# Optimization experiments

Hardware: AMD Instinct MI355X
Metric: run time of the kernel (lower is better)

The kernel has to match this reference:

```python
import jax, jax.numpy as jnp
import numpy as np

N_NODES = 4096
N_EDGES = 32768
IN_FEAT = 256
OUT_FEAT = 128
HID = 64
IN_HEAD = 64
OUT_HEAD = 5
NEG_SLOPE = 0.2
EPS = 1e-16


def setup_inputs() -> dict:
    key = jax.random.key(0)
    ks = jax.random.split(key, 12)
    x = jax.random.normal(ks[0], (N_NODES, IN_FEAT), dtype=jnp.float32)
    src = jax.random.randint(ks[1], (N_EDGES,), 0, N_NODES)
    dst = jax.random.randint(ks[2], (N_EDGES,), 0, N_NODES)
    edge_index = jnp.stack([src, dst]).astype(jnp.int64)
    s1 = 1.0 / np.sqrt(IN_FEAT)
    s2 = 1.0 / np.sqrt(HID * IN_HEAD)
    W1 = jax.random.normal(ks[3], (IN_FEAT, IN_HEAD * HID), dtype=jnp.float32) * s1
    att_src1 = jax.random.normal(ks[4], (IN_HEAD, HID), dtype=jnp.float32) * 0.1
    att_dst1 = jax.random.normal(ks[5], (IN_HEAD, HID), dtype=jnp.float32) * 0.1
    b1 = jnp.zeros((IN_HEAD * HID,), dtype=jnp.float32)
    W2 = jax.random.normal(ks[6], (IN_HEAD * HID, OUT_HEAD * OUT_FEAT), dtype=jnp.float32) * s2
    att_src2 = jax.random.normal(ks[7], (OUT_HEAD, OUT_FEAT), dtype=jnp.float32) * 0.1
    att_dst2 = jax.random.normal(ks[8], (OUT_HEAD, OUT_FEAT), dtype=jnp.float32) * 0.1
    b2 = jnp.zeros((OUT_FEAT,), dtype=jnp.float32)
    return {"x": x, "edge_index": edge_index, "W1": W1, "att_src1": att_src1,
            "att_dst1": att_dst1, "b1": b1, "W2": W2, "att_src2": att_src2,
            "att_dst2": att_dst2, "b2": b2}


def _gat_conv(x, W, att_src, att_dst, bias, src, dst, heads, out_c, concat):
    # x: [N, F_in]; returns [N, heads*out_c] (concat) or [N, out_c] (mean)
    n = x.shape[0]
    h = (x @ W).reshape(n, heads, out_c)                       # [N,H,C]
    a_src = jnp.sum(h * att_src, axis=-1)                      # [N,H]
    a_dst = jnp.sum(h * att_dst, axis=-1)                      # [N,H]
    e = jax.nn.leaky_relu(a_src[src] + a_dst[dst], NEG_SLOPE)  # [E,H]
    # segment softmax over edges grouped by destination node (PyG softmax)
    m = jax.ops.segment_max(e, dst, num_segments=n)            # [N,H]
    ex = jnp.exp(e - m[dst])
    denom = jax.ops.segment_sum(ex, dst, num_segments=n)       # [N,H]
    alpha = ex / (denom[dst] + EPS)                            # [E,H]
    out = jax.ops.segment_sum(alpha[:, :, None] * h[src], dst, num_segments=n)  # [N,H,C]
    out = out.reshape(n, heads * out_c) if concat else out.mean(axis=1)
    return out + bias


def reference(x, edge_index, W1, att_src1, att_dst1, b1, W2, att_src2, att_dst2, b2):
    n = x.shape[0]
    # PyG GATConv default: add self loops
    loop = jnp.arange(n, dtype=edge_index.dtype)
    src = jnp.concatenate([edge_index[0], loop])
    dst = jnp.concatenate([edge_index[1], loop])
    # dropout layers are identity in eval mode
    h = _gat_conv(x, W1, att_src1, att_dst1, b1, src, dst, IN_HEAD, HID, True)
    h = jax.nn.elu(h)
    h = _gat_conv(h, W2, att_src2, att_dst2, b2, src, dst, OUT_HEAD, OUT_FEAT, False)
    s = jnp.mean(h, axis=0)
    return jnp.tanh(s)
```

## Files before the change

### kernel.cpp

```cpp
#include <hip/hip_runtime.h>
#include <hip/hip_bf16.h>

#define N_NODES 4096
#define NE      32768
#define E_TOT   (NE + N_NODES)
#define IN_FEAT 256
#define HID     64
#define IN_HEAD 64
#define F1      4096
#define OUT_HEAD 5
#define OUT_FEAT 128
#define F2      640
#define NEG_SLOPE 0.2f
#define EPS_A   1e-16f

typedef __bf16 bf16;
typedef bf16 bf16x8 __attribute__((ext_vector_type(8)));
typedef bf16 bf16x4 __attribute__((ext_vector_type(4)));
typedef float f32x4 __attribute__((ext_vector_type(4)));

__device__ inline void async_cp16(bf16* lds, const bf16* g) {
    __builtin_amdgcn_global_load_lds(
        (const __attribute__((address_space(1))) unsigned int*)g,
        (__attribute__((address_space(3))) unsigned int*)lds, 16, 0, 0);
}

__global__ void hist_kernel(const int* __restrict__ edst, int* counts) {
    int e = blockIdx.x * 256 + threadIdx.x;
    if (e >= E_TOT) return;
    int d = (e < NE) ? edst[e] : (e - NE);
    atomicAdd(&counts[d], 1);
}

__global__ void scan_kernel(const int* __restrict__ counts,
                            int* __restrict__ row_start, int* __restrict__ cursor) {
    __shared__ int part[256];
    __shared__ int pre[257];
    int t = threadIdx.x;
    int base = t * 16;
    int local[16];
    int s = 0;
#pragma unroll
    for (int i = 0; i < 16; ++i) { local[i] = s; s += counts[base + i]; }
    part[t] = s;
    __syncthreads();
    if (t == 0) {
        int r = 0;
        for (int i = 0; i < 256; ++i) { pre[i] = r; r += part[i]; }
        pre[256] = r;
    }
    __syncthreads();
    int off = pre[t];
#pragma unroll
    for (int i = 0; i < 16; ++i) {
        int v = off + local[i];
        row_start[base + i] = v;
        cursor[base + i] = v;
    }
    if (t == 0) row_start[N_NODES] = pre[256];
}

__global__ void scatter_kernel(const int* __restrict__ edst,
                               int* cursor, int* __restrict__ elist) {
    int e = blockIdx.x * 256 + threadIdx.x;
    if (e >= E_TOT) return;
    int d = (e < NE) ? edst[e] : (e - NE);
    int slot = atomicAdd(&cursor[d], 1);
    elist[slot] = e;
}

#define PB_X   512
#define PB_W1  1024
#define PB_W2  2560
__global__ __launch_bounds__(256)
void prep_kernel(const float* __restrict__ x, bf16* __restrict__ xb,
                 const float* __restrict__ W1, bf16* __restrict__ W1T,
                 const float* __restrict__ W2, bf16* __restrict__ W2T,
                 const float* __restrict__ as1, const float* __restrict__ ad1,
                 bf16* __restrict__ w1s, bf16* __restrict__ w1d) {
    __shared__ float tile[32][33];
    int b = blockIdx.x, t = threadIdx.x;
    if (b < PB_X) {
        int i = b * 256 + t;
        f32x4 a = *(const f32x4*)(x + (size_t)i * 8);
        f32x4 c = *(const f32x4*)(x + (size_t)i * 8 + 4);
        bf16x8 r;
        r[0] = (bf16)a[0]; r[1] = (bf16)a[1]; r[2] = (bf16)a[2]; r[3] = (bf16)a[3];
        r[4] = (bf16)c[0]; r[5] = (bf16)c[1]; r[6] = (bf16)c[2]; r[7] = (bf16)c[3];
        *(bf16x8*)(xb + (size_t)i * 8) = r;
    } else if (b < PB_X + PB_W1 + PB_W2) {
        const float* S; bf16* D; int R, C, gx, gy;
        if (b < PB_X + PB_W1) {
            int bb = b - PB_X;
            S = W1; D = W1T; R = IN_FEAT; C = F1;
            gx = bb % (F1 / 32); gy = bb / (F1 / 32);
        } else {
            int bb = b - PB_X - PB_W1;
            S = W2; D = W2T; R = F1; C = F2;
            gx = bb % (F2 / 32); gy = bb / (F2 / 32);
        }
        int tx = t & 31, ty = t >> 5;
        int c0 = gx * 32, r0 = gy * 32;
#pragma unroll
        for (int i = 0; i < 4; ++i)
            tile[ty + i * 8][tx] = S[(size_t)(r0 + ty + i * 8) * C + c0 + tx];
        __syncthreads();
#pragma unroll
        for (int i = 0; i < 4; ++i)
            D[(size_t)(c0 + ty + i * 8) * R + r0 + tx] = (bf16)tile[tx][ty + i * 8];
    } else {
        int id = (b - PB_X - PB_W1 - PB_W2) * 256 + t;
        int k = id >> 6, h = id & 63;
        const float* wrow = W1 + (size_t)k * F1 + h * HID;
        const float* a1 = as1 + h * HID;
        const float* a2 = ad1 + h * HID;
        float s = 0.f, d = 0.f;
#pragma unroll 8
        for (int c = 0; c < HID; ++c) {
            float w = wrow[c];
            s += w * a1[c];
            d += w * a2[c];
        }
        w1s[id] = (bf16)s;
        w1d[id] = (bf16)d;
    }
}

template <int SPLITK, bool SWZ, typename TC>
__global__ __launch_bounds__(256)
void gemm128_kernel(const bf16* __restrict__ A, const bf16* __restrict__ BT,
                    TC* __restrict__ C, int M, int N, int K) {
    __shared__ bf16 As[128][64];
    __shared__ bf16 Bs[128][64];
    const int tid  = threadIdx.x;
    const int wave = tid >> 6, lane = tid & 63;
    const int quad = lane >> 4, lr = lane & 15;
    int nb, mb, zb;
    if constexpr (SWZ) {
        int bid = blockIdx.x;
        int xx = bid & 7, q = bid >> 3;
        int gp = q / 5; nb = q - gp * 5;
        int g = gp * 8 + xx;
        mb = g >> 2; zb = g & 3;
    } else {
        nb = blockIdx.x; mb = blockIdx.y; zb = blockIdx.z;
    }
    const int m0 = mb * 128, n0 = nb * 128;
    const int kchunk = K / SPLITK;
    const int kbeg = zb * kchunk;
    const int wm = (wave >> 1) * 64;
    const int wn = (wave & 1) * 64;
    TC* Cz = C + (size_t)zb * M * N;

    const int srow = lane >> 3;
    const int scol = ((lane & 7) ^ srow) * 8;
    const int xk = lr & 7;

    f32x4 acc[4][4] = {};

    for (int kk = 0; kk < kchunk; kk += 64) {
        int k0 = kbeg + kk;
#pragma unroll
        for (int c = 0; c < 4; ++c) {
            int r = wave * 32 + c * 8;
            async_cp16(&As[r][0], A + (size_t)(m0 + r + srow) * K + k0 + scol);
            async_cp16(&Bs[r][0], BT + (size_t)(n0 + r + srow) * K + k0 + scol);
        }
        __syncthreads();

#pragma unroll
        for (int ks = 0; ks < 2; ++ks) {
            int ch = ((ks * 4 + quad) ^ xk) * 8;
            bf16x8 af[4], bfr[4];
#pragma unroll
            for (int mt = 0; mt < 4; ++mt)
                af[mt] = *(const bf16x8*)(&As[wm + mt * 16 + lr][ch]);
#pragma unroll
            for (int nt = 0; nt < 4; ++nt)
                bfr[nt] = *(const bf16x8*)(&Bs[wn + nt * 16 + lr][ch]);
#pragma unroll
            for (int mt = 0; mt < 4; ++mt)
#pragma unroll
                for (int nt = 0; nt < 4; ++nt)
                    acc[mt][nt] = __builtin_amdgcn_mfma_f32_16x16x32_bf16(
                        af[mt], bfr[nt], acc[mt][nt], 0, 0, 0);
        }
        __syncthreads();
    }

#pragma unroll
    for (int mt = 0; mt < 4; ++mt)
#pragma unroll
        for (int nt = 0; nt < 4; ++nt) {
            int row0 = m0 + wm + mt * 16 + quad * 4;
            int col = n0 + wn + nt * 16 + lr;
#pragma unroll
            for (int r = 0; r < 4; ++r)
                Cz[(size_t)(row0 + r) * N + col] = (TC)acc[mt][nt][r];
        }
}

__global__ __launch_bounds__(256)
void gemv1_kernel(const float* __restrict__ x,
                  const bf16* __restrict__ w1s, const bf16* __restrict__ w1d,
                  float* __restrict__ a_src, float* __restrict__ a_dst) {
    int wave = threadIdx.x >> 6, lane = threadIdx.x & 63;
    int n = blockIdx.x * 4 + wave;
    const float* xr = x + (size_t)n * IN_FEAT;
    float s = 0.f, d = 0.f;
    for (int k0 = 0; k0 < IN_FEAT; k0 += 4) {
        f32x4 xv = *(const f32x4*)(xr + k0);
#pragma unroll
        for (int j = 0; j < 4; ++j) {
            float xs = xv[j];
            s += xs * (float)w1s[(k0 + j) * IN_HEAD + lane];
            d += xs * (float)w1d[(k0 + j) * IN_HEAD + lane];
        }
    }
    a_src[n * IN_HEAD + lane] = s;
    a_dst[n * IN_HEAD + lane] = d;
}

__global__ __launch_bounds__(64)
void agg1_kernel(const int* __restrict__ es, const int* __restrict__ row_start,
                 const int* __restrict__ elist,
                 const float* __restrict__ a_src, const float* __restrict__ a_dst,
                 const bf16* __restrict__ H1, const float* __restrict__ b1,
                 bf16* __restrict__ h_elu) {
    int bid = blockIdx.x;
    int c = bid & 7;
    int d = bid >> 3;
    int lane = threadIdx.x;
    int gh = c * 8 + (lane >> 3);
    int beg = row_start[d], deg = row_start[d + 1] - beg;
    float adst = a_dst[d * IN_HEAD + gh];
    int fbase = c * 512 + lane * 8;

    float m = -1e30f, den = 0.f;
    float acc[8] = {};
    for (int i = 0; i < deg; ++i) {
        int e = elist[beg + i];
        int s = (e < NE) ? es[e] : d;
        float l = a_src[s * IN_HEAD + gh] + adst;
        l = l > 0.f ? l : NEG_SLOPE * l;
        if (l > m + 12.f) {
            float r = __expf(m - l);
            den *= r;
#pragma unroll
            for (int k = 0; k < 8; ++k) acc[k] *= r;
            m = l;
        }
        float w = __expf(l - m);
        den += w;
        bf16x8 v = *(const bf16x8*)(H1 + (size_t)s * F1 + fbase);
#pragma unroll
        for (int k = 0; k < 8; ++k) acc[k] += w * (float)v[k];
    }
    float dinv = 1.f / (den + EPS_A);

    bf16x8 o;
#pragma unroll
    for (int j = 0; j < 8; ++j) {
        float v = acc[j] * dinv + b1[fbase + j];
        o[j] = (bf16)(v > 0.f ? v : (__expf(v) - 1.f));
    }
    *(bf16x8*)(h_elu + (size_t)d * F1 + fbase) = o;
}

__global__ __launch_bounds__(192)
void fold2_kernel(const bf16* __restrict__ Hp,
                  const float* __restrict__ as2, const float* __restrict__ ad2,
                  float* __restrict__ H2,
                  float* __restrict__ a_src, float* __restrict__ a_dst) {
    int n = blockIdx.x, t = threadIdx.x;
    if (t >= 160) return;
    int h = t >> 5;
    f32x4 sum = {};
#pragma unroll
    for (int z = 0; z < 4; ++z) {
        bf16x4 v = *(const bf16x4*)(Hp + (size_t)z * N_NODES * F2 + (size_t)n * F2 + t * 4);
        sum[0] += (float)v[0]; sum[1] += (float)v[1];
        sum[2] += (float)v[2]; sum[3] += (float)v[3];
    }
    *(f32x4*)(H2 + (size_t)n * F2 + t * 4) = sum;
    f32x4 ws = *(const f32x4*)(as2 + t * 4);
    f32x4 wd = *(const f32x4*)(ad2 + t * 4);
    float s = sum[0] * ws[0] + sum[1] * ws[1] + sum[2] * ws[2] + sum[3] * ws[3];
    float d = sum[0] * wd[0] + sum[1] * wd[1] + sum[2] * wd[2] + sum[3] * wd[3];
#pragma unroll
    for (int o = 1; o <= 16; o <<= 1) {
        s += __shfl_xor(s, o);
        d += __shfl_xor(d, o);
    }
    if ((t & 31) == 0) {
        a_src[n * OUT_HEAD + h] = s;
        a_dst[n * OUT_HEAD + h] = d;
    }
}

__global__ void stats2_kernel(const int* __restrict__ es,
                              const int* __restrict__ row_start,
                              const int* __restrict__ elist,
                              const float* __restrict__ a_src,
                              const float* __restrict__ a_dst,
                              float* __restrict__ m2, float* __restrict__ dinv2) {
    int id = blockIdx.x * 256 + threadIdx.x;
    if (id >= N_NODES * OUT_HEAD) return;
    int d = id / OUT_HEAD, h = id - d * OUT_HEAD;
    int beg = row_start[d], deg = row_start[d + 1] - beg;
    float adst = a_dst[id];
    float m = -1e30f, den = 0.f;
    for (int i = 0; i < deg; ++i) {
        int e = elist[beg + i];
        int s = (e < NE) ? es[e] : d;
        float l = a_src[s * OUT_HEAD + h] + adst;
        l = l > 0.f ? l : NEG_SLOPE * l;
        if (l > m) { den = den * __expf(m - l) + 1.f; m = l; }
        else den += __expf(l - m);
    }
    m2[id] = m;
    dinv2[id] = 1.f / (den + EPS_A);
}

__global__ void beta_kernel(const int* __restrict__ es, const int* __restrict__ ed,
                            const float* __restrict__ a_src, const float* __restrict__ a_dst,
                            const float* __restrict__ m2, const float* __restrict__ dinv2,
                            float* __restrict__ beta) {
    int id = blockIdx.x * 256 + threadIdx.x;
    if (id >= E_TOT * OUT_HEAD) return;
    int e = id / OUT_HEAD, h = id - e * OUT_HEAD;
    int s = (e < NE) ? es[e] : (e - NE);
    int d = (e < NE) ? ed[e] : (e - NE);
    float l = a_src[s * OUT_HEAD + h] + a_dst[d * OUT_HEAD + h];
    l = l > 0.f ? l : NEG_SLOPE * l;
    float alpha = __expf(l - m2[d * OUT_HEAD + h]) * dinv2[d * OUT_HEAD + h];
    atomicAdd(&beta[s * OUT_HEAD + h], alpha);
}

__global__ __launch_bounds__(256)
void wsum_kernel(const float* __restrict__ H2, const float* __restrict__ beta,
                 float* __restrict__ acc_out) {
    __shared__ float buf[F2];
    int t = threadIdx.x;
    int n0 = blockIdx.x * 32;
    int h = t >> 5;
    float a0 = 0.f, a1 = 0.f, a2 = 0.f, a3 = 0.f;
    if (t < 160) {
        for (int i = 0; i < 32; ++i) {
            int s = n0 + i;
            float bh = beta[s * OUT_HEAD + h];
            f32x4 v = *(const f32x4*)(H2 + (size_t)s * F2 + t * 4);
            a0 += bh * v[0]; a1 += bh * v[1];
            a2 += bh * v[2]; a3 += bh * v[3];
        }
        buf[t * 4 + 0] = a0; buf[t * 4 + 1] = a1;
        buf[t * 4 + 2] = a2; buf[t * 4 + 3] = a3;
    }
    __syncthreads();
    if (t < OUT_FEAT) {
        float s = 0.f;
#pragma unroll
        for (int hh = 0; hh < OUT_HEAD; ++hh) s += buf[hh * OUT_FEAT + t];
        atomicAdd(&acc_out[(blockIdx.x & 7) * OUT_FEAT + t], s);
    }
}

__global__ void tanh_kernel(const float* __restrict__ acc_out,
                            const float* __restrict__ b2, float* __restrict__ out) {
    int c = threadIdx.x;
    float tot = 0.f;
#pragma unroll
    for (int k = 0; k < 8; ++k) tot += acc_out[k * OUT_FEAT + c];
    out[c] = tanhf(tot * (1.f / (OUT_HEAD * (float)N_NODES)) + b2[c]);
}

extern "C" void kernel_launch(void* const* d_in, const int* in_sizes, int n_in,
                              void* d_out, int out_size, void* d_ws, size_t ws_size,
                              hipStream_t stream) {
    const float* x        = (const float*)d_in[0];
    const int*   ei       = (const int*)d_in[1];
    const float* W1       = (const float*)d_in[2];
    const float* att_src1 = (const float*)d_in[3];
    const float* att_dst1 = (const float*)d_in[4];
    const float* b1       = (const float*)d_in[5];
    const float* W2       = (const float*)d_in[6];
    const float* att_src2 = (const float*)d_in[7];
    const float* att_dst2 = (const float*)d_in[8];
    const float* b2       = (const float*)d_in[9];
    float* out = (float*)d_out;

    const int* esrc = ei;
    const int* edst = ei + NE;

    char* p = (char*)d_ws;
    auto bump = [&](size_t bytes) {
        void* r = (void*)p;
        p += (bytes + 255) & ~(size_t)255;
        return r;
    };
    bf16*  H1     = (bf16*)bump((size_t)N_NODES * F1 * 2);
    bf16*  h_elu  = (bf16*)bump((size_t)N_NODES * F1 * 2);
    float* H2     = (float*)bump((size_t)N_NODES * F2 * 4);
    bf16*  xb     = (bf16*)bump((size_t)N_NODES * IN_FEAT * 2);
    bf16*  W1T    = (bf16*)bump((size_t)F1 * IN_FEAT * 2);
    bf16*  W2T    = (bf16*)bump((size_t)F2 * F1 * 2);
    bf16*  w1s    = (bf16*)bump((size_t)IN_FEAT * IN_HEAD * 2);
    bf16*  w1d    = (bf16*)bump((size_t)IN_FEAT * IN_HEAD * 2);
    float* a_src1 = (float*)bump((size_t)N_NODES * IN_HEAD * 4);
    float* a_dst1 = (float*)bump((size_t)N_NODES * IN_HEAD * 4);
    float* a_src2 = (float*)bump((size_t)N_NODES * OUT_HEAD * 4);
    float* a_dst2 = (float*)bump((size_t)N_NODES * OUT_HEAD * 4);
    float* m2     = (float*)bump((size_t)N_NODES * OUT_HEAD * 4);
    float* dinv2  = (float*)bump((size_t)N_NODES * OUT_HEAD * 4);
    int*   row_start = (int*)bump((N_NODES + 1) * 4);
    int*   cursor = (int*)bump(N_NODES * 4);
    int*   elist  = (int*)bump(E_TOT * 4);
    int*   counts = (int*)bump(N_NODES * 4 + N_NODES * OUT_HEAD * 4 + 8 * OUT_FEAT * 4);
    float* beta    = (float*)((char*)counts + N_NODES * 4);
    float* acc_out = beta + N_NODES * OUT_HEAD;
    bf16* Hp = H1;

    hipMemsetAsync(counts, 0,
                   N_NODES * 4 + N_NODES * OUT_HEAD * 4 + 8 * OUT_FEAT * 4, stream);

    hist_kernel<<<(E_TOT + 255) / 256, 256, 0, stream>>>(edst, counts);
    scan_kernel<<<1, 256, 0, stream>>>(counts, row_start, cursor);
    scatter_kernel<<<(E_TOT + 255) / 256, 256, 0, stream>>>(edst, cursor, elist);

    prep_kernel<<<PB_X + PB_W1 + PB_W2 + 64, 256, 0, stream>>>(
        x, xb, W1, W1T, W2, W2T, att_src1, att_dst1, w1s, w1d);

    gemm128_kernel<1, false, bf16>
        <<<dim3(F1 / 128, N_NODES / 128, 1), 256, 0, stream>>>(
        xb, W1T, H1, N_NODES, F1, IN_FEAT);
    gemv1_kernel<<<N_NODES / 4, 256, 0, stream>>>(x, w1s, w1d, a_src1, a_dst1);
    agg1_kernel<<<N_NODES * 8, 64, 0, stream>>>(
        esrc, row_start, elist, a_src1, a_dst1, H1, b1, h_elu);

    gemm128_kernel<4, true, bf16><<<640, 256, 0, stream>>>(
        h_elu, W2T, Hp, N_NODES, F2, F1);
    fold2_kernel<<<N_NODES, 192, 0, stream>>>(
        Hp, att_src2, att_dst2, H2, a_src2, a_dst2);
    stats2_kernel<<<(N_NODES * OUT_HEAD + 255) / 256, 256, 0, stream>>>(
        esrc, row_start, elist, a_src2, a_dst2, m2, dinv2);
    beta_kernel<<<(E_TOT * OUT_HEAD + 255) / 256, 256, 0, stream>>>(
        esrc, edst, a_src2, a_dst2, m2, dinv2, beta);
    wsum_kernel<<<N_NODES / 32, 256, 0, stream>>>(H2, beta, acc_out);

    tanh_kernel<<<1, OUT_FEAT, 0, stream>>>(acc_out, b2, out);
}
```

Baseline: 252.3 us.

## Store source ids in CSR, prefetch agg1 gathers, fuse beta and tanh kernels

The scatter step now writes source node ids into the CSR list instead of edge ids, which removes one level of indirection in agg1 and stats2. agg1 adds a software pipeline that loads a_src and the H1 rows up to three edges ahead to hide gather latency. The beta kernel is folded into stats2 as a second pass over each node's edges, and the final tanh kernel is folded into wsum using a last-block ticket. Two launches go away, at the cost of more registers in agg1 and more serial per-thread work in stats2.

```diff
diff --git a/kernel.cpp b/kernel.cpp
--- a/kernel.cpp
+++ b/kernel.cpp
@@ -60,13 +60,15 @@
     if (t == 0) row_start[N_NODES] = pre[256];
 }
 
-__global__ void scatter_kernel(const int* __restrict__ edst,
-                               int* cursor, int* __restrict__ elist) {
+__global__ void scatter_kernel(const int* __restrict__ esrc,
+                               const int* __restrict__ edst,
+                               int* cursor, int* __restrict__ srclist) {
     int e = blockIdx.x * 256 + threadIdx.x;
     if (e >= E_TOT) return;
     int d = (e < NE) ? edst[e] : (e - NE);
+    int s = (e < NE) ? esrc[e] : (e - NE);
     int slot = atomicAdd(&cursor[d], 1);
-    elist[slot] = e;
+    srclist[slot] = s;
 }
 
 #define PB_X   512
@@ -222,8 +224,8 @@
 }
 
 __global__ __launch_bounds__(64)
-void agg1_kernel(const int* __restrict__ es, const int* __restrict__ row_start,
-                 const int* __restrict__ elist,
+void agg1_kernel(const int* __restrict__ row_start,
+                 const int* __restrict__ srclist,
                  const float* __restrict__ a_src, const float* __restrict__ a_dst,
                  const bf16* __restrict__ H1, const float* __restrict__ b1,
                  bf16* __restrict__ h_elu) {
@@ -235,13 +237,26 @@
     int beg = row_start[d], deg = row_start[d + 1] - beg;
     float adst = a_dst[d * IN_HEAD + gh];
     int fbase = c * 512 + lane * 8;
+    const float* asg = a_src + gh;
+
+    auto SL = [&](int i) { return srclist[beg + (i < deg ? i : deg - 1)]; };
+
+    int s0 = SL(0);
+    int s1 = SL(1);
+    float la0 = asg[(size_t)s0 * IN_HEAD];
+    bf16x8 v0 = *(const bf16x8*)(H1 + (size_t)s0 * F1 + fbase);
+    float la1 = asg[(size_t)s1 * IN_HEAD];
+    bf16x8 v1 = *(const bf16x8*)(H1 + (size_t)s1 * F1 + fbase);
+    int s2 = SL(2);
 
     float m = -1e30f, den = 0.f;
     float acc[8] = {};
     for (int i = 0; i < deg; ++i) {
-        int e = elist[beg + i];
-        int s = (e < NE) ? es[e] : d;
-        float l = a_src[s * IN_HEAD + gh] + adst;
+        int s3 = SL(i + 3);
+        float la2 = asg[(size_t)s2 * IN_HEAD];
+        bf16x8 v2 = *(const bf16x8*)(H1 + (size_t)s2 * F1 + fbase);
+
+        float l = la0 + adst;
         l = l > 0.f ? l : NEG_SLOPE * l;
         if (l > m + 12.f) {
             float r = __expf(m - l);
@@ -252,9 +267,12 @@
         }
         float w = __expf(l - m);
         den += w;
-        bf16x8 v = *(const bf16x8*)(H1 + (size_t)s * F1 + fbase);
-#pragma unroll
-        for (int k = 0; k < 8; ++k) acc[k] += w * (float)v[k];
+#pragma unroll
+        for (int k = 0; k < 8; ++k) acc[k] += w * (float)v0[k];
+
+        la0 = la1; v0 = v1;
+        la1 = la2; v1 = v2;
+        s2 = s3;
     }
     float dinv = 1.f / (den + EPS_A);
 
@@ -298,12 +316,11 @@
     }
 }
 
-__global__ void stats2_kernel(const int* __restrict__ es,
-                              const int* __restrict__ row_start,
-                              const int* __restrict__ elist,
+__global__ void stats2_kernel(const int* __restrict__ row_start,
+                              const int* __restrict__ srclist,
                               const float* __restrict__ a_src,
                               const float* __restrict__ a_dst,
-                              float* __restrict__ m2, float* __restrict__ dinv2) {
+                              float* __restrict__ beta) {
     int id = blockIdx.x * 256 + threadIdx.x;
     if (id >= N_NODES * OUT_HEAD) return;
     int d = id / OUT_HEAD, h = id - d * OUT_HEAD;
@@ -311,36 +328,27 @@
     float adst = a_dst[id];
     float m = -1e30f, den = 0.f;
     for (int i = 0; i < deg; ++i) {
-        int e = elist[beg + i];
-        int s = (e < NE) ? es[e] : d;
+        int s = srclist[beg + i];
         float l = a_src[s * OUT_HEAD + h] + adst;
         l = l > 0.f ? l : NEG_SLOPE * l;
         if (l > m) { den = den * __expf(m - l) + 1.f; m = l; }
         else den += __expf(l - m);
     }
-    m2[id] = m;
-    dinv2[id] = 1.f / (den + EPS_A);
-}
-
-__global__ void beta_kernel(const int* __restrict__ es, const int* __restrict__ ed,
-                            const float* __restrict__ a_src, const float* __restrict__ a_dst,
-                            const float* __restrict__ m2, const float* __restrict__ dinv2,
-                            float* __restrict__ beta) {
-    int id = blockIdx.x * 256 + threadIdx.x;
-    if (id >= E_TOT * OUT_HEAD) return;
-    int e = id / OUT_HEAD, h = id - e * OUT_HEAD;
-    int s = (e < NE) ? es[e] : (e - NE);
-    int d = (e < NE) ? ed[e] : (e - NE);
-    float l = a_src[s * OUT_HEAD + h] + a_dst[d * OUT_HEAD + h];
-    l = l > 0.f ? l : NEG_SLOPE * l;
-    float alpha = __expf(l - m2[d * OUT_HEAD + h]) * dinv2[d * OUT_HEAD + h];
-    atomicAdd(&beta[s * OUT_HEAD + h], alpha);
+    float dinv = 1.f / (den + EPS_A);
+    for (int i = 0; i < deg; ++i) {
+        int s = srclist[beg + i];
+        float l = a_src[s * OUT_HEAD + h] + adst;
+        l = l > 0.f ? l : NEG_SLOPE * l;
+        atomicAdd(&beta[s * OUT_HEAD + h], __expf(l - m) * dinv);
+    }
 }
 
 __global__ __launch_bounds__(256)
 void wsum_kernel(const float* __restrict__ H2, const float* __restrict__ beta,
-                 float* __restrict__ acc_out) {
+                 float* __restrict__ acc_out, const float* __restrict__ b2,
+                 float* __restrict__ out, int* __restrict__ ticket) {
     __shared__ float buf[F2];
+    __shared__ int lastblk;
     int t = threadIdx.x;
     int n0 = blockIdx.x * 32;
     int h = t >> 5;
@@ -363,15 +371,19 @@
         for (int hh = 0; hh < OUT_HEAD; ++hh) s += buf[hh * OUT_FEAT + t];
         atomicAdd(&acc_out[(blockIdx.x & 7) * OUT_FEAT + t], s);
     }
-}
-
-__global__ void tanh_kernel(const float* __restrict__ acc_out,
-                            const float* __restrict__ b2, float* __restrict__ out) {
-    int c = threadIdx.x;
-    float tot = 0.f;
-#pragma unroll
-    for (int k = 0; k < 8; ++k) tot += acc_out[k * OUT_FEAT + c];
-    out[c] = tanhf(tot * (1.f / (OUT_HEAD * (float)N_NODES)) + b2[c]);
+    __syncthreads();
+    if (t == 0) {
+        __threadfence();
+        lastblk = (atomicAdd(ticket, 1) == (int)gridDim.x - 1);
+    }
+    __syncthreads();
+    if (lastblk && t < OUT_FEAT) {
+        float tot = 0.f;
+#pragma unroll
+        for (int k = 0; k < 8; ++k)
+            tot += atomicAdd(&acc_out[k * OUT_FEAT + t], 0.0f);
+        out[t] = tanhf(tot * (1.f / (OUT_HEAD * (float)N_NODES)) + b2[t]);
+    }
 }
 
 extern "C" void kernel_launch(void* const* d_in, const int* in_sizes, int n_in,
@@ -410,22 +422,22 @@
     float* a_dst1 = (float*)bump((size_t)N_NODES * IN_HEAD * 4);
     float* a_src2 = (float*)bump((size_t)N_NODES * OUT_HEAD * 4);
     float* a_dst2 = (float*)bump((size_t)N_NODES * OUT_HEAD * 4);
-    float* m2     = (float*)bump((size_t)N_NODES * OUT_HEAD * 4);
-    float* dinv2  = (float*)bump((size_t)N_NODES * OUT_HEAD * 4);
     int*   row_start = (int*)bump((N_NODES + 1) * 4);
-    int*   cursor = (int*)bump(N_NODES * 4);
-    int*   elist  = (int*)bump(E_TOT * 4);
-    int*   counts = (int*)bump(N_NODES * 4 + N_NODES * OUT_HEAD * 4 + 8 * OUT_FEAT * 4);
+    int*   cursor  = (int*)bump(N_NODES * 4);
+    int*   srclist = (int*)bump(E_TOT * 4);
+    size_t zbytes = N_NODES * 4 + N_NODES * OUT_HEAD * 4 + 8 * OUT_FEAT * 4 + 4;
+    int*   counts = (int*)bump(zbytes);
     float* beta    = (float*)((char*)counts + N_NODES * 4);
     float* acc_out = beta + N_NODES * OUT_HEAD;
+    int*   ticket  = (int*)(acc_out + 8 * OUT_FEAT);
     bf16* Hp = H1;
 
-    hipMemsetAsync(counts, 0,
-                   N_NODES * 4 + N_NODES * OUT_HEAD * 4 + 8 * OUT_FEAT * 4, stream);
+    hipMemsetAsync(counts, 0, zbytes, stream);
 
     hist_kernel<<<(E_TOT + 255) / 256, 256, 0, stream>>>(edst, counts);
     scan_kernel<<<1, 256, 0, stream>>>(counts, row_start, cursor);
-    scatter_kernel<<<(E_TOT + 255) / 256, 256, 0, stream>>>(edst, cursor, elist);
+    scatter_kernel<<<(E_TOT + 255) / 256, 256, 0, stream>>>(
+        esrc, edst, cursor, srclist);
 
     prep_kernel<<<PB_X + PB_W1 + PB_W2 + 64, 256, 0, stream>>>(
         x, xb, W1, W1T, W2, W2T, att_src1, att_dst1, w1s, w1d);
@@ -435,17 +447,14 @@
         xb, W1T, H1, N_NODES, F1, IN_FEAT);
     gemv1_kernel<<<N_NODES / 4, 256, 0, stream>>>(x, w1s, w1d, a_src1, a_dst1);
     agg1_kernel<<<N_NODES * 8, 64, 0, stream>>>(
-        esrc, row_start, elist, a_src1, a_dst1, H1, b1, h_elu);
+        row_start, srclist, a_src1, a_dst1, H1, b1, h_elu);
 
     gemm128_kernel<4, true, bf16><<<640, 256, 0, stream>>>(
         h_elu, W2T, Hp, N_NODES, F2, F1);
     fold2_kernel<<<N_NODES, 192, 0, stream>>>(
         Hp, att_src2, att_dst2, H2, a_src2, a_dst2);
     stats2_kernel<<<(N_NODES * OUT_HEAD + 255) / 256, 256, 0, stream>>>(
-        esrc, row_start, elist, a_src2, a_dst2, m2, dinv2);
-    beta_kernel<<<(E_TOT * OUT_HEAD + 255) / 256, 256, 0, stream>>>(
-        esrc, edst, a_src2, a_dst2, m2, dinv2, beta);
-    wsum_kernel<<<N_NODES / 32, 256, 0, stream>>>(H2, beta, acc_out);
-
-    tanh_kernel<<<1, OUT_FEAT, 0, stream>>>(acc_out, b2, out);
-}
+        row_start, srclist, a_src2, a_dst2, beta);
+    wsum_kernel<<<N_NODES / 32, 256, 0, stream>>>(
+        H2, beta, acc_out, b2, out, ticket);
+}
```

Result: faster. 240.3 us (-4.8%).
